# Kernel optimization log

Hardware: AMD Instinct MI355X
Metric: run time of the kernel (lower is better)

Reference implementation:

```python
import jax, jax.numpy as jnp
import numpy as np

H, HKV, D, HID = 12, 2, 128, 1536
NGROUPS = H // HKV  # 6


def rotate_half(x):
    half = x.shape[-1] // 2
    x1, x2 = x[..., :half], x[..., half:]
    return jnp.concatenate([-x2, x1], axis=-1)


def setup_inputs() -> dict:
    key = jax.random.key(0)
    k0, k1, k2, k3 = jax.random.split(key, 4)
    B, S = 4, 2048
    NSLOTS = 16384
    x = jax.random.normal(k0, (B, S, HID), jnp.float32)
    # RoPE tables (concat-style, matches RoPE class): theta=1e6
    inv_freq = 1.0 / (1000000.0 ** (np.arange(0, D, 2, dtype=np.float64) / D))
    ang = np.outer(np.arange(S, dtype=np.float64), inv_freq)  # (S, D/2)
    cos_t = np.concatenate([np.cos(ang), np.cos(ang)], axis=-1).astype(np.float32)
    sin_t = np.concatenate([np.sin(ang), np.sin(ang)], axis=-1).astype(np.float32)
    cos = jnp.broadcast_to(jnp.asarray(cos_t)[None], (B, S, D))
    sin = jnp.broadcast_to(jnp.asarray(sin_t)[None], (B, S, D))
    kv_cache_k = jnp.zeros((NSLOTS, HKV, D), jnp.float32)
    kv_cache_v = jnp.zeros((NSLOTS, HKV, D), jnp.float32)
    slot_mapping = jnp.arange(B * S, dtype=jnp.int32)  # unique, in-range slots
    Wqkv = 0.02 * jax.random.normal(k1, (H * D + 2 * HKV * D, HID), jnp.float32)
    bqkv = 0.02 * jax.random.normal(k2, (H * D + 2 * HKV * D,), jnp.float32)
    Wo = 0.02 * jax.random.normal(k3, (HID, HID), jnp.float32)
    return {"x": x, "cos": cos, "sin": sin, "kv_cache_k": kv_cache_k,
            "kv_cache_v": kv_cache_v, "slot_mapping": slot_mapping,
            "Wqkv": Wqkv, "bqkv": bqkv, "Wo": Wo, "is_prefill": 1}


def reference(x, cos, sin, kv_cache_k, kv_cache_v, slot_mapping, Wqkv, bqkv, Wo, is_prefill):
    B, S, _ = x.shape
    qkv = x @ Wqkv.T + bqkv  # (B,S,2048)
    q_size, k_size = H * D, HKV * D
    q = qkv[..., :q_size].reshape(B, S, H, D)
    k = qkv[..., q_size:q_size + k_size].reshape(B, S, HKV, D)
    v = qkv[..., q_size + k_size:].reshape(B, S, HKV, D)
    # fused RoPE (concat-style rotate_half)
    cb, sb = cos[:, :, None, :], sin[:, :, None, :]
    q = q * cb + rotate_half(q) * sb
    k = k * cb + rotate_half(k) * sb
    # paged KV-cache store (scatter by slot)
    k_flat = k.reshape(-1, HKV, D)
    v_flat = v.reshape(-1, HKV, D)
    kc = kv_cache_k.at[slot_mapping].set(k_flat)
    vc = kv_cache_v.at[slot_mapping].set(v_flat)
    # prefill: causal GQA SDPA
    kr = jnp.repeat(k, NGROUPS, axis=2)  # (B,S,H,D)
    vr = jnp.repeat(v, NGROUPS, axis=2)
    scale = 1.0 / jnp.sqrt(jnp.float32(D))
    scores = jnp.einsum('bqhd,bkhd->bhqk', q, kr) * scale  # (B,H,S,S)
    causal = jnp.tril(jnp.ones((S, S), bool))
    scores = jnp.where(causal, scores, jnp.float32(-1e30))
    attn = jax.nn.softmax(scores, axis=-1)
    out = jnp.einsum('bhqk,bkhd->bqhd', attn, vr).reshape(B, S, HID)
    out = out @ Wo.T
    return out, kc, vc
```

## Files before the change

### kernel.cpp

```cpp
#include <hip/hip_runtime.h>
#include <hip/hip_bf16.h>
#include <stdint.h>

typedef __attribute__((ext_vector_type(8))) __bf16 bf16x8;
typedef __attribute__((ext_vector_type(4))) float f32x4;

__device__ __forceinline__ float bf2f(unsigned short u) {
  unsigned int x = ((unsigned int)u) << 16;
  float f; __builtin_memcpy(&f, &x, 4); return f;
}
__device__ __forceinline__ unsigned short f2bf(float f) {
  unsigned int x; __builtin_memcpy(&x, &f, 4);
  unsigned int r = x + 0x7fffu + ((x >> 16) & 1u);
  return (unsigned short)(r >> 16);
}
__device__ __forceinline__ unsigned int pk2(float a, float b) {
  __hip_bfloat162 h = __float22bfloat162_rn(float2{a, b});
  unsigned int u; __builtin_memcpy(&u, &h, 4); return u;
}
__device__ __forceinline__ float fmax3(float a, float b, float c) {
  return fmaxf(fmaxf(a, b), c);
}
__device__ __forceinline__ uint4 cvt8(const float* src) {
  float4 a = *(const float4*)src;
  float4 b = *(const float4*)(src + 4);
  uint4 r;
  r.x = pk2(a.x, a.y); r.y = pk2(a.z, a.w);
  r.z = pk2(b.x, b.y); r.w = pk2(b.z, b.w);
  return r;
}

__device__ __forceinline__ void gload_lds16(const unsigned short* g, unsigned short* l) {
  __builtin_amdgcn_global_load_lds(
      (const __attribute__((address_space(1))) void*)g,
      (__attribute__((address_space(3))) void*)l, 16, 0, 0);
}

__global__ __launch_bounds__(256) void cvt_all(const float* __restrict__ x,
                                               const float* __restrict__ wqkv,
                                               const float* __restrict__ wo,
                                               unsigned short* __restrict__ xb,
                                               unsigned short* __restrict__ wqkvb,
                                               unsigned short* __restrict__ wob) {
  long i = ((long)blockIdx.x * 256 + threadIdx.x) * 8;
  if (i < 12582912) { *(uint4*)(xb + i) = cvt8(x + i); return; }
  i -= 12582912;
  if (i < 3145728) { *(uint4*)(wqkvb + i) = cvt8(wqkv + i); return; }
  i -= 3145728;
  *(uint4*)(wob + i) = cvt8(wo + i);
}

template <bool OUT_F32, bool HAS_BIAS>
__global__ __launch_bounds__(256) void gemm_bt(const unsigned short* __restrict__ A,
                                               const unsigned short* __restrict__ W,
                                               const float* __restrict__ bias,
                                               void* __restrict__ Cv,
                                               int M, int N, int K) {
  __shared__ __align__(16) unsigned short sA[128 * 32];
  __shared__ __align__(16) unsigned short sB[128 * 32];
  const int tid = threadIdx.x;
  const int lane = tid & 63;
  const int w = tid >> 6;
  const long m0 = (long)blockIdx.y * 128;
  const long n0 = (long)blockIdx.x * 128;
  const int wm = (w >> 1) * 64;
  const int wn = (w & 1) * 64;
  const int fr = lane & 15, fq = lane >> 4;

  const int srow = w * 16 + (lane >> 2);
  const int scol = (lane & 3) * 8;
  const unsigned short* Ag = A + m0 * K + (long)srow * K + scol;
  const unsigned short* Wg = W + n0 * K + (long)srow * K + scol;
  const long rstep = 64L * K;
  unsigned short* sAw = sA + w * 512;
  unsigned short* sBw = sB + w * 512;

  f32x4 acc[4][4];
#pragma unroll
  for (int i = 0; i < 4; ++i)
#pragma unroll
    for (int j = 0; j < 4; ++j) acc[i][j] = f32x4{0.f, 0.f, 0.f, 0.f};

  for (int k0 = 0; k0 < K; k0 += 32) {
    __syncthreads();
    gload_lds16(Ag + k0,         sAw);
    gload_lds16(Ag + rstep + k0, sAw + 2048);
    gload_lds16(Wg + k0,         sBw);
    gload_lds16(Wg + rstep + k0, sBw + 2048);
    __syncthreads();
    bf16x8 af[4], bfr[4];
#pragma unroll
    for (int t = 0; t < 4; ++t) {
      af[t]  = *(const bf16x8*)&sA[(wm + t * 16 + fr) * 32 + fq * 8];
      bfr[t] = *(const bf16x8*)&sB[(wn + t * 16 + fr) * 32 + fq * 8];
    }
#pragma unroll
    for (int mt = 0; mt < 4; ++mt)
#pragma unroll
      for (int nt = 0; nt < 4; ++nt)
        acc[mt][nt] = __builtin_amdgcn_mfma_f32_16x16x32_bf16(af[mt], bfr[nt], acc[mt][nt], 0, 0, 0);
  }

#pragma unroll
  for (int nt = 0; nt < 4; ++nt) {
    long n = n0 + wn + nt * 16 + fr;
    float bv = HAS_BIAS ? bias[n] : 0.f;
#pragma unroll
    for (int mt = 0; mt < 4; ++mt)
#pragma unroll
      for (int r = 0; r < 4; ++r) {
        long m = m0 + wm + mt * 16 + fq * 4 + r;
        float v = acc[mt][nt][r] + bv;
        if (OUT_F32)
          ((float*)Cv)[m * N + n] = v;
        else
          ((unsigned short*)Cv)[m * N + n] = f2bf(v);
      }
  }
}

__global__ __launch_bounds__(256) void rope_scatter(unsigned short* __restrict__ qkv,
                                                    const float* __restrict__ cosb,
                                                    const float* __restrict__ sinb,
                                                    const int* __restrict__ slot_mapping,
                                                    float* __restrict__ kc,
                                                    float* __restrict__ vc,
                                                    unsigned short* __restrict__ vt) {
  const int u = blockIdx.x * 256 + threadIdx.x;
  if (u < 917504) {
    const int m = u / 112;
    const int g = u - m * 112;
    const int head = g >> 3;
    const int d0 = (g & 7) * 8;
    const int slot = slot_mapping[m];
    const size_t base = (size_t)m * 2048;
    const size_t cbase = (size_t)m * 128;
    const int off = head < 12 ? head * 128 : 1536 + (head - 12) * 128;

    union { uint4 q; unsigned short s[8]; } X1, X2, O1, O2;
    X1.q = *(const uint4*)(qkv + base + off + d0);
    X2.q = *(const uint4*)(qkv + base + off + d0 + 64);
    float c1[8], s1[8], c2[8], s2[8];
    *(float4*)&c1[0] = *(const float4*)(cosb + cbase + d0);
    *(float4*)&c1[4] = *(const float4*)(cosb + cbase + d0 + 4);
    *(float4*)&s1[0] = *(const float4*)(sinb + cbase + d0);
    *(float4*)&s1[4] = *(const float4*)(sinb + cbase + d0 + 4);
    *(float4*)&c2[0] = *(const float4*)(cosb + cbase + d0 + 64);
    *(float4*)&c2[4] = *(const float4*)(cosb + cbase + d0 + 68);
    *(float4*)&s2[0] = *(const float4*)(sinb + cbase + d0 + 64);
    *(float4*)&s2[4] = *(const float4*)(sinb + cbase + d0 + 68);

    float o1[8], o2[8];
#pragma unroll
    for (int j = 0; j < 8; ++j) {
      float x1 = bf2f(X1.s[j]), x2 = bf2f(X2.s[j]);
      o1[j] = x1 * c1[j] - x2 * s1[j];
      o2[j] = x2 * c2[j] + x1 * s2[j];
      O1.s[j] = f2bf(o1[j]);
      O2.s[j] = f2bf(o2[j]);
    }
    *(uint4*)(qkv + base + off + d0) = O1.q;
    *(uint4*)(qkv + base + off + d0 + 64) = O2.q;
    if (head >= 12) {
      float* kp = kc + (size_t)slot * 256 + (head - 12) * 128 + d0;
      *(float4*)(kp)      = *(const float4*)&o1[0];
      *(float4*)(kp + 4)  = *(const float4*)&o1[4];
      *(float4*)(kp + 64) = *(const float4*)&o2[0];
      *(float4*)(kp + 68) = *(const float4*)&o2[4];
    }
  } else {
    const int u2 = u - 917504;
    const int m = u2 & 8191;
    const int g = u2 >> 13;
    const int slot = slot_mapping[m];
    union { uint4 q; unsigned short s[8]; } V;
    V.q = *(const uint4*)(qkv + (size_t)m * 2048 + 1792 + g * 8);
    float vo[8];
#pragma unroll
    for (int j = 0; j < 8; ++j) vo[j] = bf2f(V.s[j]);
    float* vp = vc + (size_t)slot * 256 + g * 8;
    *(float4*)(vp)     = *(const float4*)&vo[0];
    *(float4*)(vp + 4) = *(const float4*)&vo[4];
    const int kvh = g >> 4;
    const int d0 = (g & 15) * 8;
    unsigned short* vtp = vt + ((size_t)((m >> 11) * 2 + kvh) * 128 + d0) * 2048 + (m & 2047);
#pragma unroll
    for (int j = 0; j < 8; ++j) vtp[(size_t)j * 2048] = V.s[j];
  }
}

__global__ __launch_bounds__(256) void attn_kernel(const unsigned short* __restrict__ qkv,
                                                   const unsigned short* __restrict__ vt,
                                                   unsigned short* __restrict__ out) {
  const int qbA = blockIdx.x;
  const int qbB = 31 - qbA;
  const int h = blockIdx.y, b = blockIdx.z;
  const int kvh = h / 6;
  __shared__ __align__(16) unsigned short sK[2][64 * 128];
  __shared__ __align__(16) unsigned short sV[2][128 * 64];
  __shared__ __align__(16) unsigned short sP[4][16 * 72];
  const int tid = threadIdx.x, lane = tid & 63, w = tid >> 6;
  const int fr = lane & 15, fq = lane >> 4;
  const float scale = 0.08838834764831845f;
  const float LOG2E = 1.44269504089f;

  bf16x8 qfA[4], qfB[4];
  {
    const unsigned short* qpA =
        qkv + ((size_t)(b * 2048 + qbA * 64 + w * 16 + fr) * 2048 + h * 128 + fq * 8);
    const unsigned short* qpB =
        qkv + ((size_t)(b * 2048 + qbB * 64 + w * 16 + fr) * 2048 + h * 128 + fq * 8);
#pragma unroll
    for (int kt = 0; kt < 4; ++kt) {
      qfA[kt] = *(const bf16x8*)(qpA + kt * 32);
      qfB[kt] = *(const bf16x8*)(qpB + kt * 32);
    }
  }
  float mA = -3.0e38f, lA = 0.f, mB = -3.0e38f, lB = 0.f;
  f32x4 accA[8], accB[8];
#pragma unroll
  for (int i = 0; i < 8; ++i) {
    accA[i] = f32x4{0.f, 0.f, 0.f, 0.f};
    accB[i] = f32x4{0.f, 0.f, 0.f, 0.f};
  }

  auto stage_K = [&](int t, int buf) {
    const size_t tok0 = (size_t)(b * 2048 + t * 64);
#pragma unroll
    for (int i = 0; i < 4; ++i) {
      int c = i * 256 + w * 64 + lane;
      int kv = c >> 4, gp = c & 15;
      int g = gp ^ (kv & 7);
      gload_lds16(qkv + (tok0 + kv) * 2048 + 1536 + kvh * 128 + g * 8,
                  &sK[buf][0] + i * 2048 + w * 512);
    }
  };
  auto stage_VT = [&](int t, int buf) {
    const size_t rowbase = (size_t)((b * 2 + kvh) * 128);
#pragma unroll
    for (int i = 0; i < 4; ++i) {
      int c = i * 256 + w * 64 + lane;
      int d = c >> 3, gp = c & 7;
      int g = gp ^ (d & 7);
      gload_lds16(vt + (rowbase + d) * 2048 + t * 64 + g * 8,
                  &sV[buf][0] + i * 2048 + w * 512);
    }
  };

  auto qk = [&](const bf16x8* qf, f32x4* s4, int cur) {
#pragma unroll
    for (int ntv = 0; ntv < 4; ++ntv) s4[ntv] = f32x4{0.f, 0.f, 0.f, 0.f};
    __builtin_amdgcn_s_setprio(1);
#pragma unroll
    for (int ntv = 0; ntv < 4; ++ntv) {
      int kvl = ntv * 16 + fr;
      int swz = kvl & 7;
#pragma unroll
      for (int kt = 0; kt < 4; ++kt) {
        bf16x8 kf = *(const bf16x8*)&sK[cur][kvl * 128 + ((kt * 4 + fq) ^ swz) * 8];
        s4[ntv] = __builtin_amdgcn_mfma_f32_16x16x32_bf16(kf, qf[kt], s4[ntv], 0, 0, 0);
      }
    }
    __builtin_amdgcn_s_setprio(0);
  };

  auto sm = [&](const f32x4* s4, float& m_i, float& l_i, f32x4* accO,
                float (&pm)[4][4], bool diag) {
    float sc[4][4];
#pragma unroll
    for (int ntv = 0; ntv < 4; ++ntv)
#pragma unroll
      for (int r = 0; r < 4; ++r) {
        float v = s4[ntv][r] * scale;
        if (diag && (ntv * 16 + fq * 4 + r > w * 16 + fr)) v = -1e30f;
        sc[ntv][r] = v;
      }
    float p0 = fmax3(sc[0][0], sc[0][1], sc[0][2]);
    float p1 = fmax3(sc[0][3], sc[1][0], sc[1][1]);
    float p2 = fmax3(sc[1][2], sc[1][3], sc[2][0]);
    float p3 = fmax3(sc[2][1], sc[2][2], sc[2][3]);
    float p4 = fmax3(sc[3][0], sc[3][1], sc[3][2]);
    float mx = fmaxf(fmax3(p0, p1, p2), fmax3(p3, p4, sc[3][3]));
    mx = fmaxf(mx, __shfl_xor(mx, 16));
    mx = fmaxf(mx, __shfl_xor(mx, 32));
    const bool keep = __all(mx <= m_i + 8.0f);
    float al = 1.f;
    if (!keep) {
      float mnew = fmaxf(m_i, mx);
      al = exp2f((m_i - mnew) * LOG2E);
      m_i = mnew;
    }
    float rs4[4];
#pragma unroll
    for (int ntv = 0; ntv < 4; ++ntv) {
#pragma unroll
      for (int r = 0; r < 4; ++r) pm[ntv][r] = exp2f((sc[ntv][r] - m_i) * LOG2E);
      rs4[ntv] = (pm[ntv][0] + pm[ntv][1]) + (pm[ntv][2] + pm[ntv][3]);
    }
    float rs = (rs4[0] + rs4[1]) + (rs4[2] + rs4[3]);
    rs += __shfl_xor(rs, 16);
    rs += __shfl_xor(rs, 32);
    if (!keep) {
      float al4[4];
#pragma unroll
      for (int r = 0; r < 4; ++r) al4[r] = __shfl(al, fq * 4 + r);
#pragma unroll
      for (int n2 = 0; n2 < 8; ++n2)
#pragma unroll
        for (int r = 0; r < 4; ++r) accO[n2][r] *= al4[r];
      l_i = l_i * al + rs;
    } else {
      l_i = l_i + rs;
    }
  };

  auto store_p = [&](const float (&pm)[4][4]) {
#pragma unroll
    for (int ntv = 0; ntv < 4; ++ntv) {
      uint2 pkd;
      pkd.x = pk2(pm[ntv][0], pm[ntv][1]);
      pkd.y = pk2(pm[ntv][2], pm[ntv][3]);
      *(uint2*)&sP[w][fr * 72 + ntv * 16 + fq * 4] = pkd;
    }
  };

  auto pv = [&](f32x4* accO, int cur) {
    __builtin_amdgcn_s_setprio(1);
#pragma unroll
    for (int kt = 0; kt < 2; ++kt) {
      bf16x8 pf = *(const bf16x8*)&sP[w][fr * 72 + kt * 32 + fq * 8];
#pragma unroll
      for (int n2 = 0; n2 < 8; ++n2) {
        int d = n2 * 16 + fr;
        bf16x8 vf = *(const bf16x8*)&sV[cur][d * 64 + (((kt * 4 + fq) ^ (d & 7)) << 3)];
        accO[n2] = __builtin_amdgcn_mfma_f32_16x16x32_bf16(pf, vf, accO[n2], 0, 0, 0);
      }
    }
    __builtin_amdgcn_s_setprio(0);
  };

  stage_K(0, 0);
  stage_VT(0, 0);
  __syncthreads();

  for (int t = 0; t <= qbB; ++t) {
    const int cur = t & 1;
    if (t < qbB) {
      stage_K(t + 1, cur ^ 1);
      stage_VT(t + 1, cur ^ 1);
    }
    if (t <= qbA) {
      f32x4 s4A[4], s4B[4];
      float pmA[4][4], pmB[4][4];
      qk(qfA, s4A, cur);
      qk(qfB, s4B, cur);
      sm(s4A, mA, lA, accA, pmA, t == qbA);
      store_p(pmA);
      sm(s4B, mB, lB, accB, pmB, t == qbB);
      pv(accA, cur);
      store_p(pmB);
      pv(accB, cur);
    } else {
      f32x4 s4B[4];
      float pmB[4][4];
      qk(qfB, s4B, cur);
      sm(s4B, mB, lB, accB, pmB, t == qbB);
      store_p(pmB);
      pv(accB, cur);
    }
    if (t < qbB) __syncthreads();
  }

  auto epilogue = [&](float l_i, const f32x4* accO, int qb) {
    float linv[4];
#pragma unroll
    for (int r = 0; r < 4; ++r) linv[r] = __shfl(l_i, fq * 4 + r);
#pragma unroll
    for (int r = 0; r < 4; ++r) {
      float inv = 1.f / linv[r];
      size_t row = (size_t)(b * 2048 + qb * 64 + w * 16 + fq * 4 + r);
#pragma unroll
      for (int n2 = 0; n2 < 8; ++n2)
        out[row * 1536 + h * 128 + n2 * 16 + fr] = f2bf(accO[n2][r] * inv);
    }
  };
  epilogue(lA, accA, qbA);
  epilogue(lB, accB, qbB);
}

extern "C" void kernel_launch(void* const* d_in, const int* in_sizes, int n_in,
                              void* d_out, int out_size, void* d_ws, size_t ws_size,
                              hipStream_t stream) {
  const float* x    = (const float*)d_in[0];
  const float* cosb = (const float*)d_in[1];
  const float* sinb = (const float*)d_in[2];
  const float* kci  = (const float*)d_in[3];
  const float* vci  = (const float*)d_in[4];
  const int* slot   = (const int*)d_in[5];
  const float* Wqkv = (const float*)d_in[6];
  const float* bqkv = (const float*)d_in[7];
  const float* Wo   = (const float*)d_in[8];

  float* out = (float*)d_out;
  float* kc  = out + (size_t)12582912;
  float* vc  = kc + (size_t)4194304;

  unsigned short* qkv_ws  = (unsigned short*)d_ws;
  unsigned short* attn_ws = qkv_ws + (size_t)16777216;
  unsigned short* xb      = attn_ws;
  unsigned short* wqkvb   = attn_ws + (size_t)12582912;
  unsigned short* wob     = wqkvb + (size_t)3145728;
  unsigned short* vt      = wqkvb;

  hipMemcpyAsync(kc, kci, (size_t)4194304 * 4, hipMemcpyDeviceToDevice, stream);
  hipMemcpyAsync(vc, vci, (size_t)4194304 * 4, hipMemcpyDeviceToDevice, stream);

  cvt_all<<<dim3(8832), 256, 0, stream>>>(x, Wqkv, Wo, xb, wqkvb, wob);
  gemm_bt<false, true><<<dim3(16, 64), 256, 0, stream>>>(
      xb, wqkvb, bqkv, qkv_ws, 8192, 2048, 1536);
  rope_scatter<<<dim3(4608), 256, 0, stream>>>(qkv_ws, cosb, sinb, slot, kc, vc, vt);
  attn_kernel<<<dim3(16, 12, 4), 256, 0, stream>>>(qkv_ws, vt, attn_ws);
  gemm_bt<true, false><<<dim3(12, 64), 256, 0, stream>>>(
      attn_ws, wob, nullptr, out, 8192, 1536, 1536);
}
```

Baseline: 547.9 us.

## Drop LDS double buffering and raise occupancy to three blocks per CU

Replaces the double-buffered K/V shared-memory staging with a single buffer that is loaded synchronously each iteration, halving LDS use. It also adds a launch_bounds minimum of three blocks per CU and serialises the A and B query-tile work to reduce live registers. The goal is higher occupancy so other waves hide memory latency, at the cost of losing explicit prefetch overlap and adding an extra barrier per iteration.

```diff
diff --git a/kernel.cpp b/kernel.cpp
--- a/kernel.cpp
+++ b/kernel.cpp
@@ -189,15 +189,15 @@
   }
 }
 
-__global__ __launch_bounds__(256) void attn_kernel(const unsigned short* __restrict__ qkv,
-                                                   const unsigned short* __restrict__ vt,
-                                                   unsigned short* __restrict__ out) {
+__global__ __launch_bounds__(256, 3) void attn_kernel(const unsigned short* __restrict__ qkv,
+                                                      const unsigned short* __restrict__ vt,
+                                                      unsigned short* __restrict__ out) {
   const int qbA = blockIdx.x;
   const int qbB = 31 - qbA;
   const int h = blockIdx.y, b = blockIdx.z;
   const int kvh = h / 6;
-  __shared__ __align__(16) unsigned short sK[2][64 * 128];
-  __shared__ __align__(16) unsigned short sV[2][128 * 64];
+  __shared__ __align__(16) unsigned short sK[64 * 128];
+  __shared__ __align__(16) unsigned short sV[128 * 64];
   __shared__ __align__(16) unsigned short sP[4][16 * 72];
   const int tid = threadIdx.x, lane = tid & 63, w = tid >> 6;
   const int fr = lane & 15, fq = lane >> 4;
@@ -224,7 +224,7 @@
     accB[i] = f32x4{0.f, 0.f, 0.f, 0.f};
   }
 
-  auto stage_K = [&](int t, int buf) {
+  auto stage_K = [&](int t) {
     const size_t tok0 = (size_t)(b * 2048 + t * 64);
 #pragma unroll
     for (int i = 0; i < 4; ++i) {
@@ -232,10 +232,10 @@
       int kv = c >> 4, gp = c & 15;
       int g = gp ^ (kv & 7);
       gload_lds16(qkv + (tok0 + kv) * 2048 + 1536 + kvh * 128 + g * 8,
-                  &sK[buf][0] + i * 2048 + w * 512);
-    }
-  };
-  auto stage_VT = [&](int t, int buf) {
+                  sK + i * 2048 + w * 512);
+    }
+  };
+  auto stage_VT = [&](int t) {
     const size_t rowbase = (size_t)((b * 2 + kvh) * 128);
 #pragma unroll
     for (int i = 0; i < 4; ++i) {
@@ -243,11 +243,11 @@
       int d = c >> 3, gp = c & 7;
       int g = gp ^ (d & 7);
       gload_lds16(vt + (rowbase + d) * 2048 + t * 64 + g * 8,
-                  &sV[buf][0] + i * 2048 + w * 512);
-    }
-  };
-
-  auto qk = [&](const bf16x8* qf, f32x4* s4, int cur) {
+                  sV + i * 2048 + w * 512);
+    }
+  };
+
+  auto qk = [&](const bf16x8* qf, f32x4* s4) {
 #pragma unroll
     for (int ntv = 0; ntv < 4; ++ntv) s4[ntv] = f32x4{0.f, 0.f, 0.f, 0.f};
     __builtin_amdgcn_s_setprio(1);
@@ -257,7 +257,7 @@
       int swz = kvl & 7;
 #pragma unroll
       for (int kt = 0; kt < 4; ++kt) {
-        bf16x8 kf = *(const bf16x8*)&sK[cur][kvl * 128 + ((kt * 4 + fq) ^ swz) * 8];
+        bf16x8 kf = *(const bf16x8*)&sK[kvl * 128 + ((kt * 4 + fq) ^ swz) * 8];
         s4[ntv] = __builtin_amdgcn_mfma_f32_16x16x32_bf16(kf, qf[kt], s4[ntv], 0, 0, 0);
       }
     }
@@ -324,7 +324,7 @@
     }
   };
 
-  auto pv = [&](f32x4* accO, int cur) {
+  auto pv = [&](f32x4* accO) {
     __builtin_amdgcn_s_setprio(1);
 #pragma unroll
     for (int kt = 0; kt < 2; ++kt) {
@@ -332,43 +332,31 @@
 #pragma unroll
       for (int n2 = 0; n2 < 8; ++n2) {
         int d = n2 * 16 + fr;
-        bf16x8 vf = *(const bf16x8*)&sV[cur][d * 64 + (((kt * 4 + fq) ^ (d & 7)) << 3)];
+        bf16x8 vf = *(const bf16x8*)&sV[d * 64 + (((kt * 4 + fq) ^ (d & 7)) << 3)];
         accO[n2] = __builtin_amdgcn_mfma_f32_16x16x32_bf16(pf, vf, accO[n2], 0, 0, 0);
       }
     }
     __builtin_amdgcn_s_setprio(0);
   };
 
-  stage_K(0, 0);
-  stage_VT(0, 0);
-  __syncthreads();
-
   for (int t = 0; t <= qbB; ++t) {
-    const int cur = t & 1;
-    if (t < qbB) {
-      stage_K(t + 1, cur ^ 1);
-      stage_VT(t + 1, cur ^ 1);
-    }
+    if (t > 0) __syncthreads();
+    stage_K(t);
+    stage_VT(t);
+    __syncthreads();
+
+    f32x4 s4[4];
+    float pm[4][4];
     if (t <= qbA) {
-      f32x4 s4A[4], s4B[4];
-      float pmA[4][4], pmB[4][4];
-      qk(qfA, s4A, cur);
-      qk(qfB, s4B, cur);
-      sm(s4A, mA, lA, accA, pmA, t == qbA);
-      store_p(pmA);
-      sm(s4B, mB, lB, accB, pmB, t == qbB);
-      pv(accA, cur);
-      store_p(pmB);
-      pv(accB, cur);
-    } else {
-      f32x4 s4B[4];
-      float pmB[4][4];
-      qk(qfB, s4B, cur);
-      sm(s4B, mB, lB, accB, pmB, t == qbB);
-      store_p(pmB);
-      pv(accB, cur);
-    }
-    if (t < qbB) __syncthreads();
+      qk(qfA, s4);
+      sm(s4, mA, lA, accA, pm, t == qbA);
+      store_p(pm);
+      pv(accA);
+    }
+    qk(qfB, s4);
+    sm(s4, mB, lB, accB, pm, t == qbB);
+    store_p(pm);
+    pv(accB);
   }
 
   auto epilogue = [&](float l_i, const f32x4* accO, int qb) {
```

Result: faster. 441.1 us (-19.5%).
